# Optimization experiments

Hardware: AMD Instinct MI355X
Metric: run time of the kernel (lower is better)

## Reference

```python
import jax, jax.numpy as jnp
import numpy as np

E, B, C = 4, 262144, 128  # edge types, tokens, feature dim

def setup_inputs() -> dict:
    key = jax.random.key(0)
    k1, k2, k3 = jax.random.split(key, 3)
    xs = jax.random.normal(k1, (E, B, C), dtype=jnp.float32)
    Ws = jax.random.normal(k2, (E, C, C), dtype=jnp.float32) * (1.0 / np.sqrt(C))
    bs = jax.random.normal(k3, (E, C), dtype=jnp.float32) * 0.01
    return {"xs": xs, "Ws": Ws, "bs": bs}

def reference(xs, Ws, bs):
    # Per-edge-type op: y_e = xs[e] @ Ws[e] + bs[e]  (Linear per from_node type)
    # Aggregation: sum over edges.
    # Fused grouped form: contract over edge axis e and input channel c in one einsum.
    out = jnp.einsum('ebc,ecd->bd', xs, Ws)          # [B, C]
    out = out + bs.sum(axis=0)                       # bias from each edge op, summed by aggregation
    return out
```

## Files before the change

kernel.cpp:

```cpp
#include <hip/hip_runtime.h>
#include <hip/hip_bf16.h>

#define N_E 4
#define N_B 262144
#define N_C 128

typedef __attribute__((ext_vector_type(8))) short bf16x8;
typedef __attribute__((ext_vector_type(4))) float f32x4;
typedef __attribute__((ext_vector_type(4))) unsigned int u32x4;

__device__ __forceinline__ unsigned pk2(float lo, float hi) {
  float2 t; t.x = lo; t.y = hi;
  __hip_bfloat162 h = __float22bfloat162_rn(t);
  union { __hip_bfloat162 h; unsigned u; } c;
  c.h = h;
  return c.u;
}

__global__ void __launch_bounds__(1024, 4)
grouped_gemm(const float* __restrict__ xs, const float* __restrict__ Ws,
             const float* __restrict__ bs, float* __restrict__ out) {
  extern __shared__ unsigned char smem[];
  unsigned short* lds_w = (unsigned short*)smem;

  const int tid  = threadIdx.x;
  const int lane = tid & 63;
  const int wave = tid >> 6;
  const int l15  = lane & 15;
  const int hi   = lane >> 4;
  const int waveRow = blockIdx.x * 256 + wave * 16;

  float bias[8];
#pragma unroll
  for (int n = 0; n < 8; ++n) {
    int d = n * 16 + l15;
    bias[n] = bs[d] + bs[128 + d] + bs[256 + d] + bs[384 + d];
  }

#pragma unroll
  for (int i = 0; i < 8; ++i) {
    int m = tid + i * 1024;
    int e = m >> 11;
    int u = (m >> 7) & 15;
    int d = m & 127;
    const float* src = Ws + e * (N_C * N_C) + u * 8 * N_C + d;
    float v[8];
#pragma unroll
    for (int j = 0; j < 8; ++j) v[j] = src[j * N_C];
    u32x4 pk;
#pragma unroll
    for (int j = 0; j < 4; ++j) pk[j] = pk2(v[2 * j], v[2 * j + 1]);
    *reinterpret_cast<u32x4*>(&lds_w[(size_t)m * 8]) = pk;
  }

  asm volatile("s_waitcnt vmcnt(0)" ::: "memory");
  __syncthreads();

  const unsigned vb = (unsigned)(waveRow + l15) * 512u + (unsigned)hi * 32u;
  const unsigned long long xbase = (unsigned long long)xs;

  f32x4 A0[4], A1[4];

#define AISSUE(c)                                                              \
  do {                                                                         \
    unsigned o;                                                                \
    asm volatile("v_add_u32 %0, %1, %2"                                        \
                 : "=v"(o)                                                     \
                 : "n"(((c) >> 2) * 134217728u + ((c) & 3) * 128u), "v"(vb));  \
    asm volatile("global_load_dwordx4 %0, %2, %3 offset:0 nt\n\t"              \
                 "global_load_dwordx4 %1, %2, %3 offset:16 nt"                 \
                 : "=&v"(A0[(c) & 3]), "=&v"(A1[(c) & 3])                      \
                 : "v"(o), "s"(xbase)                                          \
                 : "memory");                                                  \
  } while (0)

#define WAITV(n)                                          \
  do {                                                    \
    asm volatile("s_waitcnt vmcnt(" #n ")" ::: "memory"); \
    __builtin_amdgcn_sched_barrier(0);                    \
  } while (0)

  f32x4 acc[8];
#pragma unroll
  for (int n = 0; n < 8; ++n) {
    f32x4 z = {0.0f, 0.0f, 0.0f, 0.0f};
    acc[n] = z;
  }

  AISSUE(0); AISSUE(1); AISSUE(2); AISSUE(3);

#define STEP(s, w)                                                             \
  do {                                                                         \
    WAITV(w);                                                                  \
    f32x4 a0 = A0[(s) & 3];                                                    \
    f32x4 a1 = A1[(s) & 3];                                                    \
    bf16x8 afrag;                                                              \
    unsigned* au = reinterpret_cast<unsigned*>(&afrag);                        \
    au[0] = pk2(a0[0], a0[1]);                                                 \
    au[1] = pk2(a0[2], a0[3]);                                                 \
    au[2] = pk2(a1[0], a1[1]);                                                 \
    au[3] = pk2(a1[2], a1[3]);                                                 \
    if ((s) <= 11) AISSUE((s) + 4);                                            \
    const unsigned short* wb =                                                 \
        lds_w + (size_t)((((s) >> 2) * 16 + ((s) & 3) * 4 + hi) * 128 + l15) * 8; \
    _Pragma("unroll")                                                          \
    for (int n = 0; n < 8; ++n) {                                              \
      bf16x8 bfrag = *reinterpret_cast<const bf16x8*>(wb + (size_t)n * 128);   \
      acc[n] = __builtin_amdgcn_mfma_f32_16x16x32_bf16(afrag, bfrag, acc[n], 0, 0, 0); \
    }                                                                          \
  } while (0)

  STEP(0, 6);  STEP(1, 6);  STEP(2, 6);  STEP(3, 6);
  STEP(4, 6);  STEP(5, 6);  STEP(6, 6);  STEP(7, 6);
  STEP(8, 6);  STEP(9, 6);  STEP(10, 6); STEP(11, 6);
  STEP(12, 6); STEP(13, 4); STEP(14, 2); STEP(15, 0);

#undef STEP
#undef WAITV
#undef AISSUE

#pragma unroll
  for (int n = 0; n < 8; ++n) {
    int d = n * 16 + l15;
#pragma unroll
    for (int r = 0; r < 4; ++r) {
      int row = waveRow + hi * 4 + r;
      __builtin_nontemporal_store(acc[n][r] + bias[n], &out[(size_t)row * N_C + d]);
    }
  }
}

extern "C" void kernel_launch(void* const* d_in, const int* in_sizes, int n_in,
                              void* d_out, int out_size, void* d_ws, size_t ws_size,
                              hipStream_t stream) {
  const float* xs = (const float*)d_in[0];
  const float* Ws = (const float*)d_in[1];
  const float* bs = (const float*)d_in[2];
  float* out = (float*)d_out;

  const size_t smem = 131072;
  hipFuncSetAttribute((const void*)grouped_gemm,
                      hipFuncAttributeMaxDynamicSharedMemorySize, (int)smem);

  dim3 grid(N_B / 256);
  dim3 block(1024);
  hipLaunchKernelGGL(grouped_gemm, grid, block, smem, stream, xs, Ws, bs, out);
}
```

Measured before the change: 147.3 us.

## Load full contiguous 128-byte row chunks per lane with permuted K layout

Each lane now loads one contiguous 128-byte span of its x row per edge type (eight dwordx4 loads), double-buffered across edge types, instead of scattered 32-byte pieces. The weight tile in LDS is permuted along K to match this access order, which is valid because the contraction is order-independent. The bias sum moves into LDS to save registers, and the nontemporal hints are dropped from both loads and stores. Coarser prefetch granularity raises register pressure and may expose more latency at the start of each edge type.

```diff
diff --git a/kernel.cpp b/kernel.cpp
--- a/kernel.cpp
+++ b/kernel.cpp
@@ -21,7 +21,8 @@
 grouped_gemm(const float* __restrict__ xs, const float* __restrict__ Ws,
              const float* __restrict__ bs, float* __restrict__ out) {
   extern __shared__ unsigned char smem[];
-  unsigned short* lds_w = (unsigned short*)smem;
+  unsigned short* lds_w    = (unsigned short*)smem;
+  float*          lds_bias = (float*)(smem + 131072);
 
   const int tid  = threadIdx.x;
   const int lane = tid & 63;
@@ -30,20 +31,14 @@
   const int hi   = lane >> 4;
   const int waveRow = blockIdx.x * 256 + wave * 16;
 
-  float bias[8];
-#pragma unroll
-  for (int n = 0; n < 8; ++n) {
-    int d = n * 16 + l15;
-    bias[n] = bs[d] + bs[128 + d] + bs[256 + d] + bs[384 + d];
-  }
-
 #pragma unroll
   for (int i = 0; i < 8; ++i) {
     int m = tid + i * 1024;
     int e = m >> 11;
-    int u = (m >> 7) & 15;
+    int g = (m >> 7) & 15;
     int d = m & 127;
-    const float* src = Ws + e * (N_C * N_C) + u * 8 * N_C + d;
+    int kt = g >> 2, h2 = g & 3;
+    const float* src = Ws + e * (N_C * N_C) + (h2 * 32 + kt * 8) * N_C + d;
     float v[8];
 #pragma unroll
     for (int j = 0; j < 8; ++j) v[j] = src[j * N_C];
@@ -52,24 +47,35 @@
     for (int j = 0; j < 4; ++j) pk[j] = pk2(v[2 * j], v[2 * j + 1]);
     *reinterpret_cast<u32x4*>(&lds_w[(size_t)m * 8]) = pk;
   }
+  if (tid < 128) {
+    lds_bias[tid] = bs[tid] + bs[128 + tid] + bs[256 + tid] + bs[384 + tid];
+  }
 
   asm volatile("s_waitcnt vmcnt(0)" ::: "memory");
   __syncthreads();
 
-  const unsigned vb = (unsigned)(waveRow + l15) * 512u + (unsigned)hi * 32u;
+  const unsigned vb = (unsigned)(waveRow + l15) * 512u + (unsigned)hi * 128u;
   const unsigned long long xbase = (unsigned long long)xs;
 
-  f32x4 A0[4], A1[4];
+  f32x4 A[2][8];
 
-#define AISSUE(c)                                                              \
+#define AISSUE(e)                                                              \
   do {                                                                         \
     unsigned o;                                                                \
     asm volatile("v_add_u32 %0, %1, %2"                                        \
-                 : "=v"(o)                                                     \
-                 : "n"(((c) >> 2) * 134217728u + ((c) & 3) * 128u), "v"(vb));  \
-    asm volatile("global_load_dwordx4 %0, %2, %3 offset:0 nt\n\t"              \
-                 "global_load_dwordx4 %1, %2, %3 offset:16 nt"                 \
-                 : "=&v"(A0[(c) & 3]), "=&v"(A1[(c) & 3])                      \
+                 : "=v"(o) : "n"((e) * 134217728u), "v"(vb));                  \
+    asm volatile("global_load_dwordx4 %0, %8, %9 offset:0\n\t"                 \
+                 "global_load_dwordx4 %1, %8, %9 offset:16\n\t"                \
+                 "global_load_dwordx4 %2, %8, %9 offset:32\n\t"                \
+                 "global_load_dwordx4 %3, %8, %9 offset:48\n\t"                \
+                 "global_load_dwordx4 %4, %8, %9 offset:64\n\t"                \
+                 "global_load_dwordx4 %5, %8, %9 offset:80\n\t"                \
+                 "global_load_dwordx4 %6, %8, %9 offset:96\n\t"                \
+                 "global_load_dwordx4 %7, %8, %9 offset:112"                   \
+                 : "=&v"(A[(e) & 1][0]), "=&v"(A[(e) & 1][1]),                 \
+                   "=&v"(A[(e) & 1][2]), "=&v"(A[(e) & 1][3]),                 \
+                   "=&v"(A[(e) & 1][4]), "=&v"(A[(e) & 1][5]),                 \
+                   "=&v"(A[(e) & 1][6]), "=&v"(A[(e) & 1][7])                  \
                  : "v"(o), "s"(xbase)                                          \
                  : "memory");                                                  \
   } while (0)
@@ -87,22 +93,19 @@
     acc[n] = z;
   }
 
-  AISSUE(0); AISSUE(1); AISSUE(2); AISSUE(3);
-
-#define STEP(s, w)                                                             \
+#define KT(e, kt, w)                                                           \
   do {                                                                         \
     WAITV(w);                                                                  \
-    f32x4 a0 = A0[(s) & 3];                                                    \
-    f32x4 a1 = A1[(s) & 3];                                                    \
+    f32x4 a0 = A[(e) & 1][2 * (kt)];                                           \
+    f32x4 a1 = A[(e) & 1][2 * (kt) + 1];                                       \
     bf16x8 afrag;                                                              \
     unsigned* au = reinterpret_cast<unsigned*>(&afrag);                        \
     au[0] = pk2(a0[0], a0[1]);                                                 \
     au[1] = pk2(a0[2], a0[3]);                                                 \
     au[2] = pk2(a1[0], a1[1]);                                                 \
     au[3] = pk2(a1[2], a1[3]);                                                 \
-    if ((s) <= 11) AISSUE((s) + 4);                                            \
     const unsigned short* wb =                                                 \
-        lds_w + (size_t)((((s) >> 2) * 16 + ((s) & 3) * 4 + hi) * 128 + l15) * 8; \
+        lds_w + (size_t)((((e) * 4 + (kt)) * 4 + hi) * 128 + l15) * 8;         \
     _Pragma("unroll")                                                          \
     for (int n = 0; n < 8; ++n) {                                              \
       bf16x8 bfrag = *reinterpret_cast<const bf16x8*>(wb + (size_t)n * 128);   \
@@ -110,22 +113,26 @@
     }                                                                          \
   } while (0)
 
-  STEP(0, 6);  STEP(1, 6);  STEP(2, 6);  STEP(3, 6);
-  STEP(4, 6);  STEP(5, 6);  STEP(6, 6);  STEP(7, 6);
-  STEP(8, 6);  STEP(9, 6);  STEP(10, 6); STEP(11, 6);
-  STEP(12, 6); STEP(13, 4); STEP(14, 2); STEP(15, 0);
+  AISSUE(0); AISSUE(1);
+  KT(0, 0, 14); KT(0, 1, 12); KT(0, 2, 10); KT(0, 3, 8);
+  AISSUE(2);
+  KT(1, 0, 14); KT(1, 1, 12); KT(1, 2, 10); KT(1, 3, 8);
+  AISSUE(3);
+  KT(2, 0, 14); KT(2, 1, 12); KT(2, 2, 10); KT(2, 3, 8);
+  KT(3, 0, 6);  KT(3, 1, 4);  KT(3, 2, 2);  KT(3, 3, 0);
 
-#undef STEP
+#undef KT
 #undef WAITV
 #undef AISSUE
 
 #pragma unroll
   for (int n = 0; n < 8; ++n) {
     int d = n * 16 + l15;
+    float bias = lds_bias[d];
 #pragma unroll
     for (int r = 0; r < 4; ++r) {
       int row = waveRow + hi * 4 + r;
-      __builtin_nontemporal_store(acc[n][r] + bias[n], &out[(size_t)row * N_C + d]);
+      out[(size_t)row * N_C + d] = acc[n][r] + bias;
     }
   }
 }
@@ -138,7 +145,7 @@
   const float* bs = (const float*)d_in[2];
   float* out = (float*)d_out;
 
-  const size_t smem = 131072;
+  const size_t smem = 131072 + 512;
   hipFuncSetAttribute((const void*)grouped_gemm,
                       hipFuncAttributeMaxDynamicSharedMemorySize, (int)smem);
 
```

New measurement: 152.7 us. +3.7%, slower.

## Transpose MFMA operands for vectorized stores, prefetch X before weight staging

Applied to the files above, without the earlier changes.

Swaps the MFMA operand order so each lane holds four consecutive output columns of one row, which lets the epilogue write float4 stores instead of scalar nontemporal stores. The bias sum moves into LDS and is read as vectors. The first X loads are issued before the weight-to-LDS staging so their latency overlaps the staging work, and the nt hint is dropped from the X loads. LDS use grows by 512 bytes and the stores become regular instead of nontemporal.

```diff
diff --git a/kernel.cpp b/kernel.cpp
--- a/kernel.cpp
+++ b/kernel.cpp
@@ -21,7 +21,8 @@
 grouped_gemm(const float* __restrict__ xs, const float* __restrict__ Ws,
              const float* __restrict__ bs, float* __restrict__ out) {
   extern __shared__ unsigned char smem[];
-  unsigned short* lds_w = (unsigned short*)smem;
+  unsigned short* lds_w    = (unsigned short*)smem;
+  float*          lds_bias = (float*)(smem + 131072);
 
   const int tid  = threadIdx.x;
   const int lane = tid & 63;
@@ -30,12 +31,31 @@
   const int hi   = lane >> 4;
   const int waveRow = blockIdx.x * 256 + wave * 16;
 
-  float bias[8];
-#pragma unroll
-  for (int n = 0; n < 8; ++n) {
-    int d = n * 16 + l15;
-    bias[n] = bs[d] + bs[128 + d] + bs[256 + d] + bs[384 + d];
-  }
+  const unsigned vb = (unsigned)(waveRow + l15) * 512u + (unsigned)hi * 32u;
+  const unsigned long long xbase = (unsigned long long)xs;
+
+  f32x4 A0[4], A1[4];
+
+#define AISSUE(c)                                                              \
+  do {                                                                         \
+    unsigned o;                                                                \
+    asm volatile("v_add_u32 %0, %1, %2"                                        \
+                 : "=v"(o)                                                     \
+                 : "n"(((c) >> 2) * 134217728u + ((c) & 3) * 128u), "v"(vb));  \
+    asm volatile("global_load_dwordx4 %0, %2, %3 offset:0\n\t"                 \
+                 "global_load_dwordx4 %1, %2, %3 offset:16"                    \
+                 : "=&v"(A0[(c) & 3]), "=&v"(A1[(c) & 3])                      \
+                 : "v"(o), "s"(xbase)                                          \
+                 : "memory");                                                  \
+  } while (0)
+
+#define WAITV(n)                                          \
+  do {                                                    \
+    asm volatile("s_waitcnt vmcnt(" #n ")" ::: "memory"); \
+    __builtin_amdgcn_sched_barrier(0);                    \
+  } while (0)
+
+  AISSUE(0); AISSUE(1); AISSUE(2); AISSUE(3);
 
 #pragma unroll
   for (int i = 0; i < 8; ++i) {
@@ -52,33 +72,12 @@
     for (int j = 0; j < 4; ++j) pk[j] = pk2(v[2 * j], v[2 * j + 1]);
     *reinterpret_cast<u32x4*>(&lds_w[(size_t)m * 8]) = pk;
   }
+  if (tid < 128) {
+    lds_bias[tid] = bs[tid] + bs[128 + tid] + bs[256 + tid] + bs[384 + tid];
+  }
 
   asm volatile("s_waitcnt vmcnt(0)" ::: "memory");
   __syncthreads();
-
-  const unsigned vb = (unsigned)(waveRow + l15) * 512u + (unsigned)hi * 32u;
-  const unsigned long long xbase = (unsigned long long)xs;
-
-  f32x4 A0[4], A1[4];
-
-#define AISSUE(c)                                                              \
-  do {                                                                         \
-    unsigned o;                                                                \
-    asm volatile("v_add_u32 %0, %1, %2"                                        \
-                 : "=v"(o)                                                     \
-                 : "n"(((c) >> 2) * 134217728u + ((c) & 3) * 128u), "v"(vb));  \
-    asm volatile("global_load_dwordx4 %0, %2, %3 offset:0 nt\n\t"              \
-                 "global_load_dwordx4 %1, %2, %3 offset:16 nt"                 \
-                 : "=&v"(A0[(c) & 3]), "=&v"(A1[(c) & 3])                      \
-                 : "v"(o), "s"(xbase)                                          \
-                 : "memory");                                                  \
-  } while (0)
-
-#define WAITV(n)                                          \
-  do {                                                    \
-    asm volatile("s_waitcnt vmcnt(" #n ")" ::: "memory"); \
-    __builtin_amdgcn_sched_barrier(0);                    \
-  } while (0)
 
   f32x4 acc[8];
 #pragma unroll
@@ -87,15 +86,13 @@
     acc[n] = z;
   }
 
-  AISSUE(0); AISSUE(1); AISSUE(2); AISSUE(3);
-
 #define STEP(s, w)                                                             \
   do {                                                                         \
     WAITV(w);                                                                  \
     f32x4 a0 = A0[(s) & 3];                                                    \
     f32x4 a1 = A1[(s) & 3];                                                    \
-    bf16x8 afrag;                                                              \
-    unsigned* au = reinterpret_cast<unsigned*>(&afrag);                        \
+    bf16x8 xfrag;                                                              \
+    unsigned* au = reinterpret_cast<unsigned*>(&xfrag);                        \
     au[0] = pk2(a0[0], a0[1]);                                                 \
     au[1] = pk2(a0[2], a0[3]);                                                 \
     au[2] = pk2(a1[0], a1[1]);                                                 \
@@ -105,8 +102,8 @@
         lds_w + (size_t)((((s) >> 2) * 16 + ((s) & 3) * 4 + hi) * 128 + l15) * 8; \
     _Pragma("unroll")                                                          \
     for (int n = 0; n < 8; ++n) {                                              \
-      bf16x8 bfrag = *reinterpret_cast<const bf16x8*>(wb + (size_t)n * 128);   \
-      acc[n] = __builtin_amdgcn_mfma_f32_16x16x32_bf16(afrag, bfrag, acc[n], 0, 0, 0); \
+      bf16x8 wfrag = *reinterpret_cast<const bf16x8*>(wb + (size_t)n * 128);   \
+      acc[n] = __builtin_amdgcn_mfma_f32_16x16x32_bf16(wfrag, xfrag, acc[n], 0, 0, 0); \
     }                                                                          \
   } while (0)
 
@@ -119,13 +116,13 @@
 #undef WAITV
 #undef AISSUE
 
+  {
+    float* ob = out + (size_t)(waveRow + l15) * N_C + hi * 4;
 #pragma unroll
-  for (int n = 0; n < 8; ++n) {
-    int d = n * 16 + l15;
-#pragma unroll
-    for (int r = 0; r < 4; ++r) {
-      int row = waveRow + hi * 4 + r;
-      __builtin_nontemporal_store(acc[n][r] + bias[n], &out[(size_t)row * N_C + d]);
+    for (int n = 0; n < 8; ++n) {
+      f32x4 bv = *reinterpret_cast<const f32x4*>(&lds_bias[n * 16 + hi * 4]);
+      f32x4 v = acc[n] + bv;
+      *reinterpret_cast<f32x4*>(ob + n * 16) = v;
     }
   }
 }
@@ -138,7 +135,7 @@
   const float* bs = (const float*)d_in[2];
   float* out = (float*)d_out;
 
-  const size_t smem = 131072;
+  const size_t smem = 131072 + 512;
   hipFuncSetAttribute((const void*)grouped_gemm,
                       hipFuncAttributeMaxDynamicSharedMemorySize, (int)smem);
 
```

Measured after the change: 138.6 us. -5.9%, faster.
